# Kernel optimization log

Hardware: AMD Instinct MI355X
Metric: run time of the kernel (lower is better)

Reference implementation:

```python
import jax, jax.numpy as jnp
import numpy as np

EMBED_DIM = 1024
NUM_HEADS = 8
HEAD_DIM = EMBED_DIM // NUM_HEADS


def setup_inputs() -> dict:
    key = jax.random.key(0)
    k1, k2, k3, k4, k5 = jax.random.split(key, 5)
    B, N, D = 4, 2048, EMBED_DIM
    scale = 1.0 / np.sqrt(D)
    return {
        "representation": jax.random.normal(k1, (B, N, D), dtype=jnp.float32),
        "W_qkv": jax.random.normal(k2, (D, 3 * D), dtype=jnp.float32) * scale,
        "b_qkv": jnp.zeros((3 * D,), dtype=jnp.float32),
        "W_proj": jax.random.normal(k3, (D, D), dtype=jnp.float32) * scale,
        "b_proj": jnp.zeros((D,), dtype=jnp.float32),
    }


def reference(representation, W_qkv, b_qkv, W_proj, b_proj):
    B, N, D = representation.shape
    H, Hd = NUM_HEADS, HEAD_DIM
    qkv = jnp.einsum("bnd,de->bne", representation, W_qkv) + b_qkv  # [B,N,3D]
    q, k, v = jnp.split(qkv, 3, axis=-1)
    # [B,N,D] -> [B,H,N,Hd]
    split_heads = lambda x: x.reshape(B, N, H, Hd).transpose(0, 2, 1, 3)
    q, k, v = split_heads(q), split_heads(k), split_heads(v)
    dots = jnp.einsum("bhqd,bhkd->bhqk", q, k) * (Hd ** -0.5)  # [B,H,N,N]
    attn = jax.nn.softmax(dots, axis=-1)
    out = jnp.einsum("bhqk,bhkd->bhqd", attn, v)
    out = out.transpose(0, 2, 1, 3).reshape(B, N, D)  # merge heads
    return jnp.einsum("bnd,de->bne", out, W_proj) + b_proj
```

## Files before the change

### kernel.cpp

```cpp
#include <hip/hip_runtime.h>
#include <hip/hip_bf16.h>
#include <cstdint>

typedef unsigned short u16;
typedef __attribute__((ext_vector_type(8))) short short8;
typedef __attribute__((ext_vector_type(4))) float f32x4;
typedef __attribute__((ext_vector_type(4))) unsigned short u16x4;

#define NSEQ 2048
#define DMODEL 1024
#define NH 8
#define HD 128
#define KDIM 1024
#define QSCALE (0.08838834764831845f * 1.4426950408889634f)

__device__ __forceinline__ u16 f2b(float f) {
  __hip_bfloat16 h = __float2bfloat16(f);
  union { __hip_bfloat16 h; u16 u; } cv; cv.h = h; return cv.u;
}
__device__ __forceinline__ f32x4 zero4() { f32x4 z = {0.f, 0.f, 0.f, 0.f}; return z; }

__device__ __forceinline__ void gload_lds16(const u16* g, u16* l) {
  __builtin_amdgcn_global_load_lds(
      (__attribute__((address_space(1))) void*)g,
      (__attribute__((address_space(3))) void*)l, 16, 0, 0);
}

__global__ void cvt_f32_bf16(const float* __restrict__ in, u16* __restrict__ out) {
  const size_t i = ((size_t)blockIdx.x * 256 + threadIdx.x) * 8;
  f32x4 a = *(const f32x4*)&in[i];
  f32x4 b = *(const f32x4*)&in[i + 4];
  short8 o;
#pragma unroll
  for (int j = 0; j < 4; ++j) { o[j] = (short)f2b(a[j]); o[4 + j] = (short)f2b(b[j]); }
  *(short8*)&out[i] = o;
}

__global__ void transpose_k(const float* __restrict__ in, u16* __restrict__ out,
                            int R, int C) {
  __shared__ u16 tile[32][33];
  const int tx = threadIdx.x, ty = threadIdx.y;
  const int c = blockIdx.x * 32 + tx;
  const int r0 = blockIdx.y * 32;
  for (int i = ty; i < 32; i += 8) tile[i][tx] = f2b(in[(size_t)(r0 + i) * C + c]);
  __syncthreads();
  const int oc = r0 + tx;
  const int c0 = blockIdx.x * 32;
  for (int i = ty; i < 32; i += 8) out[(size_t)(c0 + i) * R + oc] = tile[tx][i];
}

template <int MODE>
__global__ __launch_bounds__(256, 3) void gemm128(
    const u16* __restrict__ A, const u16* __restrict__ Bt,
    const float* __restrict__ bias, u16* __restrict__ o0,
    u16* __restrict__ o1, u16* __restrict__ o2, float* __restrict__ of) {
  __shared__ __align__(16) u16 sA[128 * 64];
  __shared__ __align__(16) u16 sB[128 * 64];

  const int tid = threadIdx.x;
  const int lane = tid & 63;
  const int w = tid >> 6;
  const int quad = lane >> 4, ln = lane & 15;
  const int m0 = blockIdx.y * 128, n0 = blockIdx.x * 128;
  const int wm = (w >> 1) * 64, wn = (w & 1) * 64;

  f32x4 acc[4][4];
#pragma unroll
  for (int i = 0; i < 4; ++i)
#pragma unroll
    for (int j = 0; j < 4; ++j) acc[i][j] = zero4();

  const int cbase = w * 4;
  for (int kb = 0; kb < KDIM / 64; ++kb) {
    __syncthreads();
    const int k0 = kb * 64;
#pragma unroll
    for (int i = 0; i < 4; ++i) {
      int c = (cbase + i) * 64 + lane;
      int r = c >> 3, s = c & 7;
      gload_lds16(A + (size_t)(m0 + r) * KDIM + k0 + s * 8, &sA[(cbase + i) * 512]);
      gload_lds16(Bt + (size_t)(n0 + r) * KDIM + k0 + s * 8, &sB[(cbase + i) * 512]);
    }
    __syncthreads();
#pragma unroll
    for (int ks = 0; ks < 2; ++ks) {
      short8 af[4], bf[4];
      const int kc = ks * 4 + quad;
#pragma unroll
      for (int t = 0; t < 4; ++t) {
        af[t] = *(const short8*)&sA[(wm + t * 16 + ln) * 64 + kc * 8];
        bf[t] = *(const short8*)&sB[(wn + t * 16 + ln) * 64 + kc * 8];
      }
#pragma unroll
      for (int mt = 0; mt < 4; ++mt)
#pragma unroll
        for (int nt = 0; nt < 4; ++nt)
          acc[mt][nt] = __builtin_amdgcn_mfma_f32_16x16x32_bf16(
              af[mt], bf[nt], acc[mt][nt], 0, 0, 0);
    }
  }

  if (MODE == 0) {
    const int which = n0 >> 10;
    const int h = (n0 & 1023) >> 7;
#pragma unroll
    for (int mt = 0; mt < 4; ++mt) {
      const int rbase = m0 + wm + mt * 16 + quad * 4;
      const int b = rbase >> 11;
      const int n = rbase & 2047;
#pragma unroll
      for (int nt = 0; nt < 4; ++nt) {
        const int dcol = wn + nt * 16 + ln;
        const float bv = bias[n0 + dcol];
        if (which == 0) {
          u16* p = o0 + ((size_t)(b * NH + h) * NSEQ + n) * HD + dcol;
#pragma unroll
          for (int rr = 0; rr < 4; ++rr)
            p[(size_t)rr * HD] = f2b((acc[mt][nt][rr] + bv) * QSCALE);
        } else if (which == 1) {
          u16* p = o1 + ((size_t)(b * NH + h) * NSEQ + n) * HD + dcol;
#pragma unroll
          for (int rr = 0; rr < 4; ++rr)
            p[(size_t)rr * HD] = f2b(acc[mt][nt][rr] + bv);
        } else {
          u16x4 pk;
#pragma unroll
          for (int rr = 0; rr < 4; ++rr) pk[rr] = f2b(acc[mt][nt][rr] + bv);
          *(u16x4*)&o2[((size_t)(b * NH + h) * HD + dcol) * NSEQ + n] = pk;
        }
      }
    }
  } else {
#pragma unroll
    for (int mt = 0; mt < 4; ++mt) {
      const int rbase = m0 + wm + mt * 16 + quad * 4;
#pragma unroll
      for (int nt = 0; nt < 4; ++nt) {
        const int col = n0 + wn + nt * 16 + ln;
        const float bv = bias[col];
#pragma unroll
        for (int rr = 0; rr < 4; ++rr)
          of[(size_t)(rbase + rr) * DMODEL + col] = acc[mt][nt][rr] + bv;
      }
    }
  }
}

__global__ __launch_bounds__(256, 2) void attn_fused(
    const u16* __restrict__ Q, const u16* __restrict__ K,
    const u16* __restrict__ Vt, u16* __restrict__ AO) {
  __shared__ __align__(16) u16 sK[64 * 136];
  __shared__ __align__(16) u16 sV[128 * 72];
  __shared__ __align__(16) u16 sP[128 * 72];

  const int tid = threadIdx.x;
  const int w = tid >> 6, lane = tid & 63;
  const int quad = lane >> 4, ln = lane & 15;
  const int bh = blockIdx.y;
  const int q0 = blockIdx.x * 128;

  const u16* Qb = Q + ((size_t)bh * NSEQ + q0) * HD;
  const u16* Kb = K + (size_t)bh * NSEQ * HD;
  const u16* Vb = Vt + (size_t)bh * HD * NSEQ;

  short8 qf[2][4];
#pragma unroll
  for (int mt = 0; mt < 2; ++mt)
#pragma unroll
    for (int ks = 0; ks < 4; ++ks)
      qf[mt][ks] = *(const short8*)&Qb[(size_t)(w * 32 + mt * 16 + ln) * HD +
                                       ks * 32 + quad * 8];

  f32x4 o[2][8];
#pragma unroll
  for (int mt = 0; mt < 2; ++mt)
#pragma unroll
    for (int dt = 0; dt < 8; ++dt) o[mt][dt] = zero4();
  float l_part[2][4] = {{0.f, 0.f, 0.f, 0.f}, {0.f, 0.f, 0.f, 0.f}};

  short8 kreg[4], vreg[4];
#pragma unroll
  for (int i = 0; i < 4; ++i) {
    int c = i * 256 + tid;
    int rk = c >> 4, sk = c & 15;
    kreg[i] = *(const short8*)&Kb[(size_t)rk * HD + sk * 8];
    int rv = c >> 3, sv = c & 7;
    vreg[i] = *(const short8*)&Vb[(size_t)rv * NSEQ + sv * 8];
  }

  for (int kv = 0; kv < NSEQ; kv += 64) {
    __syncthreads();
#pragma unroll
    for (int i = 0; i < 4; ++i) {
      int c = i * 256 + tid;
      int rk = c >> 4, sk = c & 15;
      *(short8*)&sK[rk * 136 + sk * 8] = kreg[i];
      int rv = c >> 3, sv = c & 7;
      *(short8*)&sV[rv * 72 + sv * 8] = vreg[i];
    }
    __syncthreads();

    if (kv + 64 < NSEQ) {
#pragma unroll
      for (int i = 0; i < 4; ++i) {
        int c = i * 256 + tid;
        int rk = c >> 4, sk = c & 15;
        kreg[i] = *(const short8*)&Kb[(size_t)(kv + 64 + rk) * HD + sk * 8];
        int rv = c >> 3, sv = c & 7;
        vreg[i] = *(const short8*)&Vb[(size_t)rv * NSEQ + kv + 64 + sv * 8];
      }
    }

    f32x4 sacc[2][4];
#pragma unroll
    for (int mt = 0; mt < 2; ++mt)
#pragma unroll
      for (int nt = 0; nt < 4; ++nt) sacc[mt][nt] = zero4();
    __builtin_amdgcn_s_setprio(1);
#pragma unroll
    for (int ks = 0; ks < 4; ++ks) {
      short8 kf[4];
#pragma unroll
      for (int nt = 0; nt < 4; ++nt)
        kf[nt] = *(const short8*)&sK[(nt * 16 + ln) * 136 + ks * 32 + quad * 8];
#pragma unroll
      for (int mt = 0; mt < 2; ++mt)
#pragma unroll
        for (int nt = 0; nt < 4; ++nt)
          sacc[mt][nt] = __builtin_amdgcn_mfma_f32_16x16x32_bf16(
              qf[mt][ks], kf[nt], sacc[mt][nt], 0, 0, 0);
    }
    __builtin_amdgcn_s_setprio(0);

#pragma unroll
    for (int mt = 0; mt < 2; ++mt)
#pragma unroll
      for (int nt = 0; nt < 4; ++nt)
#pragma unroll
        for (int rr = 0; rr < 4; ++rr) {
          float p = exp2f(sacc[mt][nt][rr]);
          l_part[mt][rr] += p;
          sP[(w * 32 + mt * 16 + quad * 4 + rr) * 72 + nt * 16 + ln] = f2b(p);
        }

    __builtin_amdgcn_s_setprio(1);
#pragma unroll
    for (int ks2 = 0; ks2 < 2; ++ks2) {
      short8 pf[2], vf[8];
#pragma unroll
      for (int mt = 0; mt < 2; ++mt)
        pf[mt] = *(const short8*)&sP[(w * 32 + mt * 16 + ln) * 72 +
                                     ks2 * 32 + quad * 8];
#pragma unroll
      for (int dt = 0; dt < 8; ++dt)
        vf[dt] = *(const short8*)&sV[(dt * 16 + ln) * 72 + ks2 * 32 + quad * 8];
#pragma unroll
      for (int mt = 0; mt < 2; ++mt)
#pragma unroll
        for (int dt = 0; dt < 8; ++dt)
          o[mt][dt] = __builtin_amdgcn_mfma_f32_16x16x32_bf16(
              pf[mt], vf[dt], o[mt][dt], 0, 0, 0);
    }
    __builtin_amdgcn_s_setprio(0);
  }

  const int b = bh >> 3, h = bh & 7;
#pragma unroll
  for (int mt = 0; mt < 2; ++mt) {
    float inv[4];
#pragma unroll
    for (int rr = 0; rr < 4; ++rr) {
      float v = l_part[mt][rr];
#pragma unroll
      for (int off = 8; off >= 1; off >>= 1) v += __shfl_xor(v, off, 64);
      inv[rr] = 1.0f / v;
    }
    const int rbase = q0 + w * 32 + mt * 16 + quad * 4;
#pragma unroll
    for (int dt = 0; dt < 8; ++dt) {
      const int d = dt * 16 + ln;
#pragma unroll
      for (int rr = 0; rr < 4; ++rr)
        AO[((size_t)b * NSEQ + rbase + rr) * DMODEL + h * HD + d] =
            f2b(o[mt][dt][rr] * inv[rr]);
    }
  }
}

extern "C" void kernel_launch(void* const* d_in, const int* in_sizes, int n_in,
                              void* d_out, int out_size, void* d_ws, size_t ws_size,
                              hipStream_t stream) {
  const float* X = (const float*)d_in[0];
  const float* Wqkv = (const float*)d_in[1];
  const float* bqkv = (const float*)d_in[2];
  const float* Wproj = (const float*)d_in[3];
  const float* bproj = (const float*)d_in[4];
  float* out = (float*)d_out;

  const size_t NEED_BYTES =
      2ull * (8388608  + 3072 * 1024 + 1024 * 1024 + 3 * 8388608 + 8388608);
  if (ws_size < NEED_BYTES) return;

  u16* ws = (u16*)d_ws;
  u16* Xb = ws;
  u16* WqkvT = Xb + 8388608;
  u16* WprojT = WqkvT + 3072 * 1024;
  u16* Qb = WprojT + 1024 * 1024;
  u16* Kb = Qb + 8388608;
  u16* Vtb = Kb + 8388608;
  u16* AO = Vtb + 8388608;

  cvt_f32_bf16<<<8388608 / (256 * 8), 256, 0, stream>>>(X, Xb);
  transpose_k<<<dim3(3072 / 32, 1024 / 32), dim3(32, 8), 0, stream>>>(Wqkv, WqkvT, 1024, 3072);
  transpose_k<<<dim3(1024 / 32, 1024 / 32), dim3(32, 8), 0, stream>>>(Wproj, WprojT, 1024, 1024);
  gemm128<0><<<dim3(3072 / 128, 8192 / 128), 256, 0, stream>>>(
      Xb, WqkvT, bqkv, Qb, Kb, Vtb, nullptr);
  attn_fused<<<dim3(2048 / 128, 32), 256, 0, stream>>>(Qb, Kb, Vtb, AO);
  gemm128<1><<<dim3(1024 / 128, 8192 / 128), 256, 0, stream>>>(
      AO, WprojT, bproj, nullptr, nullptr, nullptr, out);
}
```

Measured before the change: 290.9 us.

## Double-buffer K/V via direct global-to-LDS loads and keep P in registers

Replaces the register-staged K/V prefetch with global_load_lds into double-buffered, XOR-swizzled shared memory, which removes one barrier and the register-to-LDS copy. It also computes S transposed (K as the A operand) so the softmax probabilities land in registers already in the MFMA operand layout, which removes the sP shared-memory round trip. The row-sum reduction is reworked to match the new layout. Shared memory use changes (two K/V buffers, no sP), and the correctness of the swizzle and row permutation is a risk.

```diff
diff --git a/kernel.cpp b/kernel.cpp
--- a/kernel.cpp
+++ b/kernel.cpp
@@ -24,6 +24,10 @@
   __builtin_amdgcn_global_load_lds(
       (__attribute__((address_space(1))) void*)g,
       (__attribute__((address_space(3))) void*)l, 16, 0, 0);
+}
+
+__device__ __forceinline__ int LK(int r) {
+  return (r & 0x23) | ((r & 0x0C) << 1) | ((r & 0x10) >> 2);
 }
 
 __global__ void cvt_f32_bf16(const float* __restrict__ in, u16* __restrict__ out) {
@@ -149,9 +153,8 @@
 __global__ __launch_bounds__(256, 2) void attn_fused(
     const u16* __restrict__ Q, const u16* __restrict__ K,
     const u16* __restrict__ Vt, u16* __restrict__ AO) {
-  __shared__ __align__(16) u16 sK[64 * 136];
-  __shared__ __align__(16) u16 sV[128 * 72];
-  __shared__ __align__(16) u16 sP[128 * 72];
+  __shared__ __align__(16) u16 sK[2][64 * 128];
+  __shared__ __align__(16) u16 sV[2][128 * 64];
 
   const int tid = threadIdx.x;
   const int w = tid >> 6, lane = tid & 63;
@@ -163,6 +166,16 @@
   const u16* Kb = K + (size_t)bh * NSEQ * HD;
   const u16* Vb = Vt + (size_t)bh * HD * NSEQ;
 
+  int gk_off[4], gv_off[4];
+#pragma unroll
+  for (int j = 0; j < 4; ++j) {
+    const int c = (w * 4 + j) * 64 + lane;
+    const int rk = c >> 4, sk_ = c & 15;
+    gk_off[j] = LK(rk) * HD + (sk_ ^ (rk & 7)) * 8;
+    const int rv = c >> 3, sv_ = c & 7;
+    gv_off[j] = rv * NSEQ + (sv_ ^ (rv & 7)) * 8;
+  }
+
   short8 qf[2][4];
 #pragma unroll
   for (int mt = 0; mt < 2; ++mt)
@@ -176,105 +189,96 @@
   for (int mt = 0; mt < 2; ++mt)
 #pragma unroll
     for (int dt = 0; dt < 8; ++dt) o[mt][dt] = zero4();
-  float l_part[2][4] = {{0.f, 0.f, 0.f, 0.f}, {0.f, 0.f, 0.f, 0.f}};
-
-  short8 kreg[4], vreg[4];
-#pragma unroll
-  for (int i = 0; i < 4; ++i) {
-    int c = i * 256 + tid;
-    int rk = c >> 4, sk = c & 15;
-    kreg[i] = *(const short8*)&Kb[(size_t)rk * HD + sk * 8];
-    int rv = c >> 3, sv = c & 7;
-    vreg[i] = *(const short8*)&Vb[(size_t)rv * NSEQ + sv * 8];
-  }
-
+  float l_part[2] = {0.f, 0.f};
+
+#pragma unroll
+  for (int j = 0; j < 4; ++j) {
+    gload_lds16(Kb + gk_off[j], &sK[0][(w * 4 + j) * 512]);
+    gload_lds16(Vb + gv_off[j], &sV[0][(w * 4 + j) * 512]);
+  }
+
+  int cur = 0;
   for (int kv = 0; kv < NSEQ; kv += 64) {
     __syncthreads();
-#pragma unroll
-    for (int i = 0; i < 4; ++i) {
-      int c = i * 256 + tid;
-      int rk = c >> 4, sk = c & 15;
-      *(short8*)&sK[rk * 136 + sk * 8] = kreg[i];
-      int rv = c >> 3, sv = c & 7;
-      *(short8*)&sV[rv * 72 + sv * 8] = vreg[i];
-    }
-    __syncthreads();
 
     if (kv + 64 < NSEQ) {
 #pragma unroll
-      for (int i = 0; i < 4; ++i) {
-        int c = i * 256 + tid;
-        int rk = c >> 4, sk = c & 15;
-        kreg[i] = *(const short8*)&Kb[(size_t)(kv + 64 + rk) * HD + sk * 8];
-        int rv = c >> 3, sv = c & 7;
-        vreg[i] = *(const short8*)&Vb[(size_t)rv * NSEQ + kv + 64 + sv * 8];
-      }
-    }
-
-    f32x4 sacc[2][4];
-#pragma unroll
-    for (int mt = 0; mt < 2; ++mt)
-#pragma unroll
-      for (int nt = 0; nt < 4; ++nt) sacc[mt][nt] = zero4();
+      for (int j = 0; j < 4; ++j) {
+        gload_lds16(Kb + (size_t)(kv + 64) * HD + gk_off[j],
+                    &sK[cur ^ 1][(w * 4 + j) * 512]);
+        gload_lds16(Vb + (kv + 64) + gv_off[j],
+                    &sV[cur ^ 1][(w * 4 + j) * 512]);
+      }
+    }
+
+    f32x4 sacc[4][2];
+#pragma unroll
+    for (int n = 0; n < 4; ++n)
+#pragma unroll
+      for (int mt = 0; mt < 2; ++mt) sacc[n][mt] = zero4();
     __builtin_amdgcn_s_setprio(1);
 #pragma unroll
     for (int ks = 0; ks < 4; ++ks) {
       short8 kf[4];
 #pragma unroll
-      for (int nt = 0; nt < 4; ++nt)
-        kf[nt] = *(const short8*)&sK[(nt * 16 + ln) * 136 + ks * 32 + quad * 8];
-#pragma unroll
-      for (int mt = 0; mt < 2; ++mt)
-#pragma unroll
-        for (int nt = 0; nt < 4; ++nt)
-          sacc[mt][nt] = __builtin_amdgcn_mfma_f32_16x16x32_bf16(
-              qf[mt][ks], kf[nt], sacc[mt][nt], 0, 0, 0);
+      for (int n = 0; n < 4; ++n)
+        kf[n] = *(const short8*)
+            &sK[cur][(n * 16 + ln) * 128 + ((((ks << 2) | quad)) ^ (ln & 7)) * 8];
+#pragma unroll
+      for (int n = 0; n < 4; ++n)
+#pragma unroll
+        for (int mt = 0; mt < 2; ++mt)
+          sacc[n][mt] = __builtin_amdgcn_mfma_f32_16x16x32_bf16(
+              kf[n], qf[mt][ks], sacc[n][mt], 0, 0, 0);
     }
     __builtin_amdgcn_s_setprio(0);
 
+    short8 pf[2][2];
 #pragma unroll
     for (int mt = 0; mt < 2; ++mt)
 #pragma unroll
-      for (int nt = 0; nt < 4; ++nt)
-#pragma unroll
-        for (int rr = 0; rr < 4; ++rr) {
-          float p = exp2f(sacc[mt][nt][rr]);
-          l_part[mt][rr] += p;
-          sP[(w * 32 + mt * 16 + quad * 4 + rr) * 72 + nt * 16 + ln] = f2b(p);
-        }
+      for (int ks2 = 0; ks2 < 2; ++ks2) {
+        short8 pv;
+#pragma unroll
+        for (int hf = 0; hf < 2; ++hf)
+#pragma unroll
+          for (int rr = 0; rr < 4; ++rr) {
+            float p = exp2f(sacc[ks2 * 2 + hf][mt][rr]);
+            l_part[mt] += p;
+            pv[hf * 4 + rr] = (short)f2b(p);
+          }
+        pf[mt][ks2] = pv;
+      }
 
     __builtin_amdgcn_s_setprio(1);
 #pragma unroll
     for (int ks2 = 0; ks2 < 2; ++ks2) {
-      short8 pf[2], vf[8];
-#pragma unroll
-      for (int mt = 0; mt < 2; ++mt)
-        pf[mt] = *(const short8*)&sP[(w * 32 + mt * 16 + ln) * 72 +
-                                     ks2 * 32 + quad * 8];
+      short8 vf[8];
 #pragma unroll
       for (int dt = 0; dt < 8; ++dt)
-        vf[dt] = *(const short8*)&sV[(dt * 16 + ln) * 72 + ks2 * 32 + quad * 8];
+        vf[dt] = *(const short8*)
+            &sV[cur][(dt * 16 + ln) * 64 + ((((ks2 << 2) | quad)) ^ (ln & 7)) * 8];
 #pragma unroll
       for (int mt = 0; mt < 2; ++mt)
 #pragma unroll
         for (int dt = 0; dt < 8; ++dt)
           o[mt][dt] = __builtin_amdgcn_mfma_f32_16x16x32_bf16(
-              pf[mt], vf[dt], o[mt][dt], 0, 0, 0);
+              pf[mt][ks2], vf[dt], o[mt][dt], 0, 0, 0);
     }
     __builtin_amdgcn_s_setprio(0);
+    cur ^= 1;
   }
 
   const int b = bh >> 3, h = bh & 7;
 #pragma unroll
   for (int mt = 0; mt < 2; ++mt) {
+    float v = l_part[mt];
+    v += __shfl_xor(v, 16, 64);
+    v += __shfl_xor(v, 32, 64);
     float inv[4];
 #pragma unroll
-    for (int rr = 0; rr < 4; ++rr) {
-      float v = l_part[mt][rr];
-#pragma unroll
-      for (int off = 8; off >= 1; off >>= 1) v += __shfl_xor(v, off, 64);
-      inv[rr] = 1.0f / v;
-    }
+    for (int rr = 0; rr < 4; ++rr)
+      inv[rr] = 1.0f / __shfl(v, quad * 4 + rr, 64);
     const int rbase = q0 + w * 32 + mt * 16 + quad * 4;
 #pragma unroll
     for (int dt = 0; dt < 8; ++dt) {
```

Measured after the change: 273.7 us. 5.9% less time.
